# Performance work log

Measured on AMD Instinct MI355X. Metric: run time of the kernel, lower is better.

The kernel has to match this reference:

```python
import jax, jax.numpy as jnp
import numpy as np

N = 8192
IN_DIM = 512
OUT_DIM = 64
ALPHA = 0.2  # LeakyReLU negative slope
NEG_FILL = -9e15


def setup_inputs() -> dict:
    key = jax.random.key(0)
    k1, k2, k3, k4 = jax.random.split(key, 4)
    features = jax.random.normal(k1, (N, IN_DIM), dtype=jnp.float32)
    adj = jax.random.randint(k2, (N, N), 0, 2, dtype=jnp.int32)
    # xavier_normal with gain 1.414 ~ sqrt(2)
    W = jax.random.normal(k3, (IN_DIM, OUT_DIM), dtype=jnp.float32) * (1.414 * np.sqrt(2.0 / (IN_DIM + OUT_DIM)))
    a = jax.random.normal(k4, (2 * OUT_DIM, 1), dtype=jnp.float32) * (1.414 * np.sqrt(2.0 / (2 * OUT_DIM + 1)))
    return {"features": features, "adj": adj, "W": W, "a": a}


def reference(features, adj, W, a):
    h = features @ W                      # [N, OUT_DIM]
    h1 = h @ a[:OUT_DIM, :]               # [N, 1]
    h2 = h @ a[OUT_DIM:, :]               # [N, 1]
    e = h1 + h2.T                         # [N, N] broadcast add
    e = jnp.where(e > 0, e, ALPHA * e)    # LeakyReLU
    scores = jnp.where(adj > 0, e, NEG_FILL)
    attention = jax.nn.softmax(scores, axis=-1)
    out = attention @ h                   # [N, OUT_DIM]
    out = jax.nn.elu(out)                 # concat=True branch
    return out
```

## Files before the change

kernel.cpp:

```cpp
#include <hip/hip_runtime.h>
#include <hip/hip_bf16.h>

#define N 8192
#define IN_DIM 512
#define OUT_DIM 64
#define ALPHA 0.2f
#define LOG2E 1.44269504f

typedef __hip_bfloat16 bf16;
typedef __attribute__((ext_vector_type(8))) short bf16x8;
typedef __attribute__((ext_vector_type(4))) float f32x4;
typedef __attribute__((ext_vector_type(4))) int   int4v;
typedef __attribute__((ext_vector_type(4))) float float4v;

__device__ __forceinline__ float u2f(unsigned short u) {
    union { unsigned int i; float f; } c; c.i = ((unsigned int)u) << 16; return c.f;
}

__device__ __forceinline__ uint2 splitpack2(float f0, float f1) {
    unsigned u0 = __float_as_uint(f0), u1 = __float_as_uint(f1);
    unsigned h0 = u0 & 0xFFFF0000u, h1 = u1 & 0xFFFF0000u;
    float l0 = f0 - __uint_as_float(h0);
    float l1 = f1 - __uint_as_float(h1);
    uint2 r;
    r.x = (h0 >> 16) | h1;
    r.y = (__float_as_uint(l0) >> 16) | (__float_as_uint(l1) & 0xFFFF0000u);
    return r;
}

__device__ __forceinline__ bf16x8 as_bf16x8(int a, int b, int c, int d) {
    union { int4v i; bf16x8 b; } u;
    u.i = (int4v){a, b, c, d};
    return u.b;
}

__global__ void k_sniff(const unsigned short* __restrict__ feat_u16, int* __restrict__ flag) {
    int lane = threadIdx.x;
    float v = u2f(feat_u16[2 * lane]);
    float av = fabsf(v);
    int ok = (v == 0.f) || (av > 1e-8f && av < 1e8f);
    unsigned long long m = __ballot(ok);
    if (lane == 0) *flag = (__popcll(m) >= 48) ? 1 : 0;
}

__global__ __launch_bounds__(256) void k_prep(const void* __restrict__ Wv,
                                              const int* __restrict__ flag,
                                              unsigned short* __restrict__ WT_hi,
                                              unsigned short* __restrict__ WT_lo) {
    int idx = blockIdx.x * 256 + threadIdx.x;
    int k = idx >> 6, c = idx & 63;
    float w = (*flag) ? u2f(((const unsigned short*)Wv)[idx]) : ((const float*)Wv)[idx];
    unsigned u = __float_as_uint(w);
    unsigned hi = u & 0xFFFF0000u;
    float lo = w - __uint_as_float(hi);
    WT_hi[c * IN_DIM + k] = (unsigned short)(hi >> 16);
    WT_lo[c * IN_DIM + k] = (unsigned short)(__float_as_uint(lo) >> 16);
}

__global__ __launch_bounds__(64) void k_h(const void* __restrict__ featv,
                                          const unsigned short* __restrict__ WT_hi,
                                          const unsigned short* __restrict__ WT_lo,
                                          const void* __restrict__ av,
                                          const int* __restrict__ flag,
                                          float* __restrict__ h1,
                                          float* __restrict__ h2,
                                          unsigned short* __restrict__ hT_hi,
                                          unsigned short* __restrict__ hT_lo) {
    const int lane = threadIdx.x & 63;
    const int rsub = lane & 15;
    const int g = lane >> 4;
    const int wrow0 = blockIdx.x * 16;
    const int isbf = *flag;

    f32x4 acc0 = {0.f,0.f,0.f,0.f}, acc1 = {0.f,0.f,0.f,0.f};
    f32x4 acc2 = {0.f,0.f,0.f,0.f}, acc3 = {0.f,0.f,0.f,0.f};

    for (int k0 = 0; k0 < IN_DIM; k0 += 32) {
        const int ka = k0 + g * 8;
        bf16x8 Ah, Al;
        if (isbf) {
            Ah = *(const bf16x8*)((const unsigned short*)featv + (size_t)(wrow0 + rsub) * IN_DIM + ka);
            Al = as_bf16x8(0, 0, 0, 0);
        } else {
            const float* fp = (const float*)featv + (size_t)(wrow0 + rsub) * IN_DIM + ka;
            float4v f0 = *(const float4v*)fp;
            float4v f1 = *(const float4v*)(fp + 4);
            uint2 q0 = splitpack2(f0[0], f0[1]);
            uint2 q1 = splitpack2(f0[2], f0[3]);
            uint2 q2 = splitpack2(f1[0], f1[1]);
            uint2 q3 = splitpack2(f1[2], f1[3]);
            Ah = as_bf16x8((int)q0.x, (int)q1.x, (int)q2.x, (int)q3.x);
            Al = as_bf16x8((int)q0.y, (int)q1.y, (int)q2.y, (int)q3.y);
        }
        const unsigned short* wh = WT_hi + (size_t)rsub * IN_DIM + ka;
        const unsigned short* wl = WT_lo + (size_t)rsub * IN_DIM + ka;
        bf16x8 B0h = *(const bf16x8*)(wh);
        bf16x8 B1h = *(const bf16x8*)(wh + 16 * IN_DIM);
        bf16x8 B2h = *(const bf16x8*)(wh + 32 * IN_DIM);
        bf16x8 B3h = *(const bf16x8*)(wh + 48 * IN_DIM);
        bf16x8 B0l = *(const bf16x8*)(wl);
        bf16x8 B1l = *(const bf16x8*)(wl + 16 * IN_DIM);
        bf16x8 B2l = *(const bf16x8*)(wl + 32 * IN_DIM);
        bf16x8 B3l = *(const bf16x8*)(wl + 48 * IN_DIM);

        acc0 = __builtin_amdgcn_mfma_f32_16x16x32_bf16(Ah, B0h, acc0, 0, 0, 0);
        acc1 = __builtin_amdgcn_mfma_f32_16x16x32_bf16(Ah, B1h, acc1, 0, 0, 0);
        acc2 = __builtin_amdgcn_mfma_f32_16x16x32_bf16(Ah, B2h, acc2, 0, 0, 0);
        acc3 = __builtin_amdgcn_mfma_f32_16x16x32_bf16(Ah, B3h, acc3, 0, 0, 0);
        acc0 = __builtin_amdgcn_mfma_f32_16x16x32_bf16(Ah, B0l, acc0, 0, 0, 0);
        acc1 = __builtin_amdgcn_mfma_f32_16x16x32_bf16(Ah, B1l, acc1, 0, 0, 0);
        acc2 = __builtin_amdgcn_mfma_f32_16x16x32_bf16(Ah, B2l, acc2, 0, 0, 0);
        acc3 = __builtin_amdgcn_mfma_f32_16x16x32_bf16(Ah, B3l, acc3, 0, 0, 0);
        acc0 = __builtin_amdgcn_mfma_f32_16x16x32_bf16(Al, B0h, acc0, 0, 0, 0);
        acc1 = __builtin_amdgcn_mfma_f32_16x16x32_bf16(Al, B1h, acc1, 0, 0, 0);
        acc2 = __builtin_amdgcn_mfma_f32_16x16x32_bf16(Al, B2h, acc2, 0, 0, 0);
        acc3 = __builtin_amdgcn_mfma_f32_16x16x32_bf16(Al, B3h, acc3, 0, 0, 0);
    }

    {
        uint2 s01, s23;
        size_t off;
        s01 = splitpack2(acc0[0], acc0[1]); s23 = splitpack2(acc0[2], acc0[3]);
        off = (size_t)(0 * 16 + rsub) * N + wrow0 + g * 4;
        { uint2 ph; ph.x = s01.x; ph.y = s23.x; *(uint2*)(hT_hi + off) = ph; }
        { uint2 pl; pl.x = s01.y; pl.y = s23.y; *(uint2*)(hT_lo + off) = pl; }
        s01 = splitpack2(acc1[0], acc1[1]); s23 = splitpack2(acc1[2], acc1[3]);
        off = (size_t)(1 * 16 + rsub) * N + wrow0 + g * 4;
        { uint2 ph; ph.x = s01.x; ph.y = s23.x; *(uint2*)(hT_hi + off) = ph; }
        { uint2 pl; pl.x = s01.y; pl.y = s23.y; *(uint2*)(hT_lo + off) = pl; }
        s01 = splitpack2(acc2[0], acc2[1]); s23 = splitpack2(acc2[2], acc2[3]);
        off = (size_t)(2 * 16 + rsub) * N + wrow0 + g * 4;
        { uint2 ph; ph.x = s01.x; ph.y = s23.x; *(uint2*)(hT_hi + off) = ph; }
        { uint2 pl; pl.x = s01.y; pl.y = s23.y; *(uint2*)(hT_lo + off) = pl; }
        s01 = splitpack2(acc3[0], acc3[1]); s23 = splitpack2(acc3[2], acc3[3]);
        off = (size_t)(3 * 16 + rsub) * N + wrow0 + g * 4;
        { uint2 ph; ph.x = s01.x; ph.y = s23.x; *(uint2*)(hT_hi + off) = ph; }
        { uint2 pl; pl.x = s01.y; pl.y = s23.y; *(uint2*)(hT_lo + off) = pl; }
    }

    const float* af = (const float*)av;
    const unsigned short* au = (const unsigned short*)av;
    float a10 = isbf ? u2f(au[rsub])      : af[rsub];
    float a11 = isbf ? u2f(au[16 + rsub]) : af[16 + rsub];
    float a12 = isbf ? u2f(au[32 + rsub]) : af[32 + rsub];
    float a13 = isbf ? u2f(au[48 + rsub]) : af[48 + rsub];
    float a20 = isbf ? u2f(au[64 + rsub])  : af[64 + rsub];
    float a21 = isbf ? u2f(au[80 + rsub])  : af[80 + rsub];
    float a22 = isbf ? u2f(au[96 + rsub])  : af[96 + rsub];
    float a23 = isbf ? u2f(au[112 + rsub]) : af[112 + rsub];
    float s1r[4], s2r[4];
#pragma unroll
    for (int r = 0; r < 4; ++r) {
        s1r[r] = acc0[r] * a10 + acc1[r] * a11 + acc2[r] * a12 + acc3[r] * a13;
        s2r[r] = acc0[r] * a20 + acc1[r] * a21 + acc2[r] * a22 + acc3[r] * a23;
    }
#pragma unroll
    for (int off = 8; off; off >>= 1) {
#pragma unroll
        for (int r = 0; r < 4; ++r) {
            s1r[r] += __shfl_xor(s1r[r], off);
            s2r[r] += __shfl_xor(s2r[r], off);
        }
    }
    if (rsub < 4) {
        float v1 = rsub == 0 ? s1r[0] : rsub == 1 ? s1r[1] : rsub == 2 ? s1r[2] : s1r[3];
        float v2 = rsub == 0 ? s2r[0] : rsub == 1 ? s2r[1] : rsub == 2 ? s2r[2] : s2r[3];
        h1[wrow0 + g * 4 + rsub] = v1;
        h2[wrow0 + g * 4 + rsub] = v2;
    }
}

__global__ void k_h2max(const float* __restrict__ h2, float* __restrict__ h2max) {
    __shared__ float red[4];
    float m = -3e38f;
    for (int i = threadIdx.x; i < N; i += 256) m = fmaxf(m, h2[i]);
#pragma unroll
    for (int off = 32; off; off >>= 1) m = fmaxf(m, __shfl_xor(m, off));
    if ((threadIdx.x & 63) == 0) red[threadIdx.x >> 6] = m;
    __syncthreads();
    if (threadIdx.x == 0) *h2max = fmaxf(fmaxf(red[0], red[1]), fmaxf(red[2], red[3]));
}

__global__ __launch_bounds__(256, 4) void k_attn(const int* __restrict__ adj,
                                                 const float* __restrict__ h1,
                                                 const float* __restrict__ h2,
                                                 const unsigned short* __restrict__ hT_hi,
                                                 const unsigned short* __restrict__ hT_lo,
                                                 const float* __restrict__ h2max,
                                                 float* __restrict__ pacc,
                                                 float* __restrict__ plner,
                                                 int klen) {
    __shared__ float accs[4][16][64];
    __shared__ float lred[4][16];

    const int wave = threadIdx.x >> 6;
    const int lane = threadIdx.x & 63;
    const int rsub = lane & 15;
    const int g = lane >> 4;
    const int row0 = blockIdx.x * 16;
    const int row = row0 + rsub;
    const int kbid = blockIdx.y;

    const float h1r = h1[row];
    float M = h1r + *h2max;
    M = fmaxf(M, ALPHA * M);
    const float c0 = -M * LOG2E;

    f32x4 acc0 = {0.f,0.f,0.f,0.f}, acc1 = {0.f,0.f,0.f,0.f};
    f32x4 acc2 = {0.f,0.f,0.f,0.f}, acc3 = {0.f,0.f,0.f,0.f};
    float lacc = 0.f;

    const size_t arow = (size_t)row * N;
    const unsigned short* bph = hT_hi + (size_t)rsub * N;
    const unsigned short* bpl = hT_lo + (size_t)rsub * N;

    const int kbeg = kbid * klen + wave * (klen >> 2);
    const int kend = kbeg + (klen >> 2);
    for (int k0 = kbeg; k0 < kend; k0 += 32) {
        const int kb = k0 + g * 8;
        int4v aj0 = *(const int4v*)(adj + arow + kb);
        int4v aj1 = *(const int4v*)(adj + arow + kb + 4);
        float4v hA = *(const float4v*)(h2 + kb);
        float4v hB = *(const float4v*)(h2 + kb + 4);

        float w[8];
#pragma unroll
        for (int j = 0; j < 4; ++j) {
            float t = h1r + hA[j];
            float s = fmaxf(t, ALPHA * t);
            float e = exp2f(fmaf(s, LOG2E, c0));
            w[j] = aj0[j] > 0 ? e : 0.f;
        }
#pragma unroll
        for (int j = 0; j < 4; ++j) {
            float t = h1r + hB[j];
            float s = fmaxf(t, ALPHA * t);
            float e = exp2f(fmaf(s, LOG2E, c0));
            w[4 + j] = aj1[j] > 0 ? e : 0.f;
        }
#pragma unroll
        for (int j = 0; j < 8; ++j) lacc += w[j];

        uint2 p0 = splitpack2(w[0], w[1]);
        uint2 p1 = splitpack2(w[2], w[3]);
        uint2 p2 = splitpack2(w[4], w[5]);
        uint2 p3 = splitpack2(w[6], w[7]);
        bf16x8 Ahi = as_bf16x8((int)p0.x, (int)p1.x, (int)p2.x, (int)p3.x);
        bf16x8 Alo = as_bf16x8((int)p0.y, (int)p1.y, (int)p2.y, (int)p3.y);

        const unsigned short* bh = bph + kb;
        const unsigned short* bl = bpl + kb;
        bf16x8 B0h = *(const bf16x8*)(bh);
        bf16x8 B1h = *(const bf16x8*)(bh + 16 * (size_t)N);
        bf16x8 B2h = *(const bf16x8*)(bh + 32 * (size_t)N);
        bf16x8 B3h = *(const bf16x8*)(bh + 48 * (size_t)N);
        bf16x8 B0l = *(const bf16x8*)(bl);
        bf16x8 B1l = *(const bf16x8*)(bl + 16 * (size_t)N);
        bf16x8 B2l = *(const bf16x8*)(bl + 32 * (size_t)N);
        bf16x8 B3l = *(const bf16x8*)(bl + 48 * (size_t)N);

        acc0 = __builtin_amdgcn_mfma_f32_16x16x32_bf16(Ahi, B0h, acc0, 0, 0, 0);
        acc1 = __builtin_amdgcn_mfma_f32_16x16x32_bf16(Ahi, B1h, acc1, 0, 0, 0);
        acc2 = __builtin_amdgcn_mfma_f32_16x16x32_bf16(Ahi, B2h, acc2, 0, 0, 0);
        acc3 = __builtin_amdgcn_mfma_f32_16x16x32_bf16(Ahi, B3h, acc3, 0, 0, 0);
        acc0 = __builtin_amdgcn_mfma_f32_16x16x32_bf16(Ahi, B0l, acc0, 0, 0, 0);
        acc1 = __builtin_amdgcn_mfma_f32_16x16x32_bf16(Ahi, B1l, acc1, 0, 0, 0);
        acc2 = __builtin_amdgcn_mfma_f32_16x16x32_bf16(Ahi, B2l, acc2, 0, 0, 0);
        acc3 = __builtin_amdgcn_mfma_f32_16x16x32_bf16(Ahi, B3l, acc3, 0, 0, 0);
        acc0 = __builtin_amdgcn_mfma_f32_16x16x32_bf16(Alo, B0h, acc0, 0, 0, 0);
        acc1 = __builtin_amdgcn_mfma_f32_16x16x32_bf16(Alo, B1h, acc1, 0, 0, 0);
        acc2 = __builtin_amdgcn_mfma_f32_16x16x32_bf16(Alo, B2h, acc2, 0, 0, 0);
        acc3 = __builtin_amdgcn_mfma_f32_16x16x32_bf16(Alo, B3h, acc3, 0, 0, 0);
    }

    lacc += __shfl_xor(lacc, 16);
    lacc += __shfl_xor(lacc, 32);
    if (g == 0) lred[wave][rsub] = lacc;

#pragma unroll
    for (int r = 0; r < 4; ++r) {
        accs[wave][g * 4 + r][rsub]      = acc0[r];
        accs[wave][g * 4 + r][16 + rsub] = acc1[r];
        accs[wave][g * 4 + r][32 + rsub] = acc2[r];
        accs[wave][g * 4 + r][48 + rsub] = acc3[r];
    }
    __syncthreads();

    float* pa = pacc + (size_t)kbid * (N * OUT_DIM);
#pragma unroll
    for (int p = 0; p < 4; ++p) {
        int idx = p * 256 + threadIdx.x;
        int rl = idx >> 6, col = idx & 63;
        float v = accs[0][rl][col] + accs[1][rl][col] + accs[2][rl][col] + accs[3][rl][col];
        pa[(size_t)(row0 + rl) * OUT_DIM + col] = v;
        if (col == 0)
            plner[(size_t)kbid * N + row0 + rl] = lred[0][rl] + lred[1][rl] + lred[2][rl] + lred[3][rl];
    }
}

__global__ __launch_bounds__(256) void k_out(const float* __restrict__ pacc,
                                             const float* __restrict__ plner,
                                             const int* __restrict__ flag,
                                             void* __restrict__ outv,
                                             int nkb) {
    int idx = blockIdx.x * 256 + threadIdx.x;
    int row = idx >> 6;
    float v = 0.f, l = 0.f;
    for (int kb = 0; kb < nkb; ++kb) {
        v += pacc[(size_t)kb * (N * OUT_DIM) + idx];
        l += plner[(size_t)kb * N + row];
    }
    float o = l > 0.f ? v / l : 0.f;
    o = o > 0.f ? o : exp2f(o * LOG2E) - 1.f;
    if (*flag) ((bf16*)outv)[idx] = __float2bfloat16(o);
    else       ((float*)outv)[idx] = o;
}

extern "C" void kernel_launch(void* const* d_in, const int* in_sizes, int n_in,
                              void* d_out, int out_size, void* d_ws, size_t ws_size,
                              hipStream_t stream) {
    const void* feat = d_in[0];
    const int* adj = (const int*)d_in[1];
    const void* W = d_in[2];
    const void* a = d_in[3];

    char* ws = (char*)d_ws;
    int*   flag   = (int*)(ws);
    float* h2max  = (float*)(ws + 256);
    float* h1     = (float*)(ws + 4096);
    float* h2     = (float*)(ws + 36864);
    unsigned short* hT_hi = (unsigned short*)(ws + 69632);
    unsigned short* hT_lo = (unsigned short*)(ws + 69632 + 1048576);
    unsigned short* WT_hi = (unsigned short*)(ws + 2166784);
    unsigned short* WT_lo = (unsigned short*)(ws + 2166784 + 65536);
    char* dynbase = ws + 2297856;

    size_t cap = ws_size ? ws_size : ((size_t)1 << 30);
    int nkb = 4;
    while (nkb > 1) {
        size_t need = 2297856 + (size_t)nkb * ((size_t)N * OUT_DIM * 4 + (size_t)N * 4);
        if (need <= cap) break;
        nkb >>= 1;
    }
    float* pacc  = (float*)dynbase;
    float* plner = (float*)(dynbase + (size_t)nkb * N * OUT_DIM * 4);

    hipLaunchKernelGGL(k_sniff, dim3(1), dim3(64), 0, stream,
                       (const unsigned short*)feat, flag);
    hipLaunchKernelGGL(k_prep, dim3((IN_DIM * OUT_DIM) / 256), dim3(256), 0, stream,
                       W, flag, WT_hi, WT_lo);
    hipLaunchKernelGGL(k_h, dim3(N / 16), dim3(64), 0, stream,
                       feat, WT_hi, WT_lo, a, flag, h1, h2, hT_hi, hT_lo);
    hipLaunchKernelGGL(k_h2max, dim3(1), dim3(256), 0, stream, h2, h2max);
    hipLaunchKernelGGL(k_attn, dim3(N / 16, nkb), dim3(256), 0, stream,
                       adj, h1, h2, hT_hi, hT_lo, h2max, pacc, plner, N / nkb);
    hipLaunchKernelGGL(k_out, dim3((N * OUT_DIM) / 256), dim3(256), 0, stream,
                       pacc, plner, flag, d_out, nkb);
}
```

Baseline: 510.7 us.

## Tile attention over 64 rows per block and fuse h2 max via atomics

Each k_attn block now covers 64 rows (four 16-row MFMA tiles) instead of 16. The hT B-fragments and h2 loads are reused across the four row tiles, which cuts redundant B traffic by four. The separate k_h2max launch is removed; k_h computes the h2 max with an order-preserving encoded atomicMax, and h1/h2 are stored prescaled by log2e. The wave partial sums are reduced serially into a padded shared tile. Occupancy is lowered (launch bounds 256,2) to fit 64 accumulator vectors, and the K split is raised to 8, which adds partial-sum traffic in k_out.

```diff
diff --git a/kernel.cpp b/kernel.cpp
--- a/kernel.cpp
+++ b/kernel.cpp
@@ -34,6 +34,14 @@
     return u.b;
 }
 
+__device__ __forceinline__ unsigned fenc(float f) {
+    unsigned u = __float_as_uint(f);
+    return (u & 0x80000000u) ? ~u : (u | 0x80000000u);
+}
+__device__ __forceinline__ float fdec(unsigned e) {
+    return (e & 0x80000000u) ? __uint_as_float(e & 0x7FFFFFFFu) : __uint_as_float(~e);
+}
+
 __global__ void k_sniff(const unsigned short* __restrict__ feat_u16, int* __restrict__ flag) {
     int lane = threadIdx.x;
     float v = u2f(feat_u16[2 * lane]);
@@ -46,7 +54,9 @@
 __global__ __launch_bounds__(256) void k_prep(const void* __restrict__ Wv,
                                               const int* __restrict__ flag,
                                               unsigned short* __restrict__ WT_hi,
-                                              unsigned short* __restrict__ WT_lo) {
+                                              unsigned short* __restrict__ WT_lo,
+                                              unsigned* __restrict__ h2enc) {
+    if (blockIdx.x == 0 && threadIdx.x == 0) *h2enc = fenc(-3e38f);
     int idx = blockIdx.x * 256 + threadIdx.x;
     int k = idx >> 6, c = idx & 63;
     float w = (*flag) ? u2f(((const unsigned short*)Wv)[idx]) : ((const float*)Wv)[idx];
@@ -65,7 +75,8 @@
                                           float* __restrict__ h1,
                                           float* __restrict__ h2,
                                           unsigned short* __restrict__ hT_hi,
-                                          unsigned short* __restrict__ hT_lo) {
+                                          unsigned short* __restrict__ hT_lo,
+                                          unsigned* __restrict__ h2enc) {
     const int lane = threadIdx.x & 63;
     const int rsub = lane & 15;
     const int g = lane >> 4;
@@ -162,55 +173,54 @@
             s2r[r] += __shfl_xor(s2r[r], off);
         }
     }
+    float wm = fmaxf(fmaxf(s2r[0], s2r[1]), fmaxf(s2r[2], s2r[3])) * LOG2E;
+#pragma unroll
+    for (int off = 32; off; off >>= 1) wm = fmaxf(wm, __shfl_xor(wm, off));
+    if (lane == 0) atomicMax(h2enc, fenc(wm));
+
     if (rsub < 4) {
         float v1 = rsub == 0 ? s1r[0] : rsub == 1 ? s1r[1] : rsub == 2 ? s1r[2] : s1r[3];
         float v2 = rsub == 0 ? s2r[0] : rsub == 1 ? s2r[1] : rsub == 2 ? s2r[2] : s2r[3];
-        h1[wrow0 + g * 4 + rsub] = v1;
-        h2[wrow0 + g * 4 + rsub] = v2;
-    }
-}
-
-__global__ void k_h2max(const float* __restrict__ h2, float* __restrict__ h2max) {
-    __shared__ float red[4];
-    float m = -3e38f;
-    for (int i = threadIdx.x; i < N; i += 256) m = fmaxf(m, h2[i]);
-#pragma unroll
-    for (int off = 32; off; off >>= 1) m = fmaxf(m, __shfl_xor(m, off));
-    if ((threadIdx.x & 63) == 0) red[threadIdx.x >> 6] = m;
-    __syncthreads();
-    if (threadIdx.x == 0) *h2max = fmaxf(fmaxf(red[0], red[1]), fmaxf(red[2], red[3]));
-}
-
-__global__ __launch_bounds__(256, 4) void k_attn(const int* __restrict__ adj,
+        h1[wrow0 + g * 4 + rsub] = v1 * LOG2E;
+        h2[wrow0 + g * 4 + rsub] = v2 * LOG2E;
+    }
+}
+
+__global__ __launch_bounds__(256, 2) void k_attn(const int* __restrict__ adj,
                                                  const float* __restrict__ h1,
                                                  const float* __restrict__ h2,
                                                  const unsigned short* __restrict__ hT_hi,
                                                  const unsigned short* __restrict__ hT_lo,
-                                                 const float* __restrict__ h2max,
+                                                 const unsigned* __restrict__ h2enc,
                                                  float* __restrict__ pacc,
                                                  float* __restrict__ plner,
                                                  int klen) {
-    __shared__ float accs[4][16][64];
-    __shared__ float lred[4][16];
+    __shared__ float accs[64][66];
+    __shared__ float lredL[4][64];
 
     const int wave = threadIdx.x >> 6;
     const int lane = threadIdx.x & 63;
     const int rsub = lane & 15;
     const int g = lane >> 4;
-    const int row0 = blockIdx.x * 16;
-    const int row = row0 + rsub;
+    const int row0 = blockIdx.x * 64;
     const int kbid = blockIdx.y;
 
-    const float h1r = h1[row];
-    float M = h1r + *h2max;
-    M = fmaxf(M, ALPHA * M);
-    const float c0 = -M * LOG2E;
-
-    f32x4 acc0 = {0.f,0.f,0.f,0.f}, acc1 = {0.f,0.f,0.f,0.f};
-    f32x4 acc2 = {0.f,0.f,0.f,0.f}, acc3 = {0.f,0.f,0.f,0.f};
-    float lacc = 0.f;
-
-    const size_t arow = (size_t)row * N;
+    const float h2m = fdec(*h2enc);
+    float h1r[4], c0[4];
+#pragma unroll
+    for (int mt = 0; mt < 4; ++mt) {
+        h1r[mt] = h1[row0 + mt * 16 + rsub];
+        float u = h1r[mt] + h2m;
+        c0[mt] = -fmaxf(u, ALPHA * u);
+    }
+
+    f32x4 acc[4][4];
+#pragma unroll
+    for (int mt = 0; mt < 4; ++mt)
+#pragma unroll
+        for (int ct = 0; ct < 4; ++ct) acc[mt][ct] = (f32x4){0.f, 0.f, 0.f, 0.f};
+    float lacc[4] = {0.f, 0.f, 0.f, 0.f};
+
     const unsigned short* bph = hT_hi + (size_t)rsub * N;
     const unsigned short* bpl = hT_lo + (size_t)rsub * N;
 
@@ -218,35 +228,6 @@
     const int kend = kbeg + (klen >> 2);
     for (int k0 = kbeg; k0 < kend; k0 += 32) {
         const int kb = k0 + g * 8;
-        int4v aj0 = *(const int4v*)(adj + arow + kb);
-        int4v aj1 = *(const int4v*)(adj + arow + kb + 4);
-        float4v hA = *(const float4v*)(h2 + kb);
-        float4v hB = *(const float4v*)(h2 + kb + 4);
-
-        float w[8];
-#pragma unroll
-        for (int j = 0; j < 4; ++j) {
-            float t = h1r + hA[j];
-            float s = fmaxf(t, ALPHA * t);
-            float e = exp2f(fmaf(s, LOG2E, c0));
-            w[j] = aj0[j] > 0 ? e : 0.f;
-        }
-#pragma unroll
-        for (int j = 0; j < 4; ++j) {
-            float t = h1r + hB[j];
-            float s = fmaxf(t, ALPHA * t);
-            float e = exp2f(fmaf(s, LOG2E, c0));
-            w[4 + j] = aj1[j] > 0 ? e : 0.f;
-        }
-#pragma unroll
-        for (int j = 0; j < 8; ++j) lacc += w[j];
-
-        uint2 p0 = splitpack2(w[0], w[1]);
-        uint2 p1 = splitpack2(w[2], w[3]);
-        uint2 p2 = splitpack2(w[4], w[5]);
-        uint2 p3 = splitpack2(w[6], w[7]);
-        bf16x8 Ahi = as_bf16x8((int)p0.x, (int)p1.x, (int)p2.x, (int)p3.x);
-        bf16x8 Alo = as_bf16x8((int)p0.y, (int)p1.y, (int)p2.y, (int)p3.y);
 
         const unsigned short* bh = bph + kb;
         const unsigned short* bl = bpl + kb;
@@ -259,43 +240,97 @@
         bf16x8 B2l = *(const bf16x8*)(bl + 32 * (size_t)N);
         bf16x8 B3l = *(const bf16x8*)(bl + 48 * (size_t)N);
 
-        acc0 = __builtin_amdgcn_mfma_f32_16x16x32_bf16(Ahi, B0h, acc0, 0, 0, 0);
-        acc1 = __builtin_amdgcn_mfma_f32_16x16x32_bf16(Ahi, B1h, acc1, 0, 0, 0);
-        acc2 = __builtin_amdgcn_mfma_f32_16x16x32_bf16(Ahi, B2h, acc2, 0, 0, 0);
-        acc3 = __builtin_amdgcn_mfma_f32_16x16x32_bf16(Ahi, B3h, acc3, 0, 0, 0);
-        acc0 = __builtin_amdgcn_mfma_f32_16x16x32_bf16(Ahi, B0l, acc0, 0, 0, 0);
-        acc1 = __builtin_amdgcn_mfma_f32_16x16x32_bf16(Ahi, B1l, acc1, 0, 0, 0);
-        acc2 = __builtin_amdgcn_mfma_f32_16x16x32_bf16(Ahi, B2l, acc2, 0, 0, 0);
-        acc3 = __builtin_amdgcn_mfma_f32_16x16x32_bf16(Ahi, B3l, acc3, 0, 0, 0);
-        acc0 = __builtin_amdgcn_mfma_f32_16x16x32_bf16(Alo, B0h, acc0, 0, 0, 0);
-        acc1 = __builtin_amdgcn_mfma_f32_16x16x32_bf16(Alo, B1h, acc1, 0, 0, 0);
-        acc2 = __builtin_amdgcn_mfma_f32_16x16x32_bf16(Alo, B2h, acc2, 0, 0, 0);
-        acc3 = __builtin_amdgcn_mfma_f32_16x16x32_bf16(Alo, B3h, acc3, 0, 0, 0);
-    }
-
-    lacc += __shfl_xor(lacc, 16);
-    lacc += __shfl_xor(lacc, 32);
-    if (g == 0) lred[wave][rsub] = lacc;
-
-#pragma unroll
-    for (int r = 0; r < 4; ++r) {
-        accs[wave][g * 4 + r][rsub]      = acc0[r];
-        accs[wave][g * 4 + r][16 + rsub] = acc1[r];
-        accs[wave][g * 4 + r][32 + rsub] = acc2[r];
-        accs[wave][g * 4 + r][48 + rsub] = acc3[r];
+        float4v hA = *(const float4v*)(h2 + kb);
+        float4v hB = *(const float4v*)(h2 + kb + 4);
+
+#pragma unroll
+        for (int mt = 0; mt < 4; ++mt) {
+            const size_t arow = (size_t)(row0 + mt * 16 + rsub) * N + kb;
+            int4v aj0 = *(const int4v*)(adj + arow);
+            int4v aj1 = *(const int4v*)(adj + arow + 4);
+
+            float w[8];
+#pragma unroll
+            for (int j = 0; j < 4; ++j) {
+                float u = h1r[mt] + hA[j];
+                float s = fmaxf(u, ALPHA * u);
+                float e = exp2f(s + c0[mt]);
+                w[j] = aj0[j] > 0 ? e : 0.f;
+            }
+#pragma unroll
+            for (int j = 0; j < 4; ++j) {
+                float u = h1r[mt] + hB[j];
+                float s = fmaxf(u, ALPHA * u);
+                float e = exp2f(s + c0[mt]);
+                w[4 + j] = aj1[j] > 0 ? e : 0.f;
+            }
+#pragma unroll
+            for (int j = 0; j < 8; ++j) lacc[mt] += w[j];
+
+            uint2 p0 = splitpack2(w[0], w[1]);
+            uint2 p1 = splitpack2(w[2], w[3]);
+            uint2 p2 = splitpack2(w[4], w[5]);
+            uint2 p3 = splitpack2(w[6], w[7]);
+            bf16x8 Ahi = as_bf16x8((int)p0.x, (int)p1.x, (int)p2.x, (int)p3.x);
+            bf16x8 Alo = as_bf16x8((int)p0.y, (int)p1.y, (int)p2.y, (int)p3.y);
+
+            acc[mt][0] = __builtin_amdgcn_mfma_f32_16x16x32_bf16(Ahi, B0h, acc[mt][0], 0, 0, 0);
+            acc[mt][1] = __builtin_amdgcn_mfma_f32_16x16x32_bf16(Ahi, B1h, acc[mt][1], 0, 0, 0);
+            acc[mt][2] = __builtin_amdgcn_mfma_f32_16x16x32_bf16(Ahi, B2h, acc[mt][2], 0, 0, 0);
+            acc[mt][3] = __builtin_amdgcn_mfma_f32_16x16x32_bf16(Ahi, B3h, acc[mt][3], 0, 0, 0);
+            acc[mt][0] = __builtin_amdgcn_mfma_f32_16x16x32_bf16(Ahi, B0l, acc[mt][0], 0, 0, 0);
+            acc[mt][1] = __builtin_amdgcn_mfma_f32_16x16x32_bf16(Ahi, B1l, acc[mt][1], 0, 0, 0);
+            acc[mt][2] = __builtin_amdgcn_mfma_f32_16x16x32_bf16(Ahi, B2l, acc[mt][2], 0, 0, 0);
+            acc[mt][3] = __builtin_amdgcn_mfma_f32_16x16x32_bf16(Ahi, B3l, acc[mt][3], 0, 0, 0);
+            acc[mt][0] = __builtin_amdgcn_mfma_f32_16x16x32_bf16(Alo, B0h, acc[mt][0], 0, 0, 0);
+            acc[mt][1] = __builtin_amdgcn_mfma_f32_16x16x32_bf16(Alo, B1h, acc[mt][1], 0, 0, 0);
+            acc[mt][2] = __builtin_amdgcn_mfma_f32_16x16x32_bf16(Alo, B2h, acc[mt][2], 0, 0, 0);
+            acc[mt][3] = __builtin_amdgcn_mfma_f32_16x16x32_bf16(Alo, B3h, acc[mt][3], 0, 0, 0);
+        }
+    }
+
+#pragma unroll
+    for (int mt = 0; mt < 4; ++mt) {
+        float l = lacc[mt];
+        l += __shfl_xor(l, 16);
+        l += __shfl_xor(l, 32);
+        if (g == 0) lredL[wave][mt * 16 + rsub] = l;
+    }
+
+    if (wave == 0) {
+#pragma unroll
+        for (int mt = 0; mt < 4; ++mt)
+#pragma unroll
+            for (int ct = 0; ct < 4; ++ct)
+#pragma unroll
+                for (int r = 0; r < 4; ++r)
+                    accs[mt * 16 + g * 4 + r][ct * 16 + rsub] = acc[mt][ct][r];
     }
     __syncthreads();
+#pragma unroll
+    for (int w2 = 1; w2 < 4; ++w2) {
+        if (wave == w2) {
+#pragma unroll
+            for (int mt = 0; mt < 4; ++mt)
+#pragma unroll
+                for (int ct = 0; ct < 4; ++ct)
+#pragma unroll
+                    for (int r = 0; r < 4; ++r)
+                        accs[mt * 16 + g * 4 + r][ct * 16 + rsub] += acc[mt][ct][r];
+        }
+        __syncthreads();
+    }
 
     float* pa = pacc + (size_t)kbid * (N * OUT_DIM);
 #pragma unroll
-    for (int p = 0; p < 4; ++p) {
+    for (int p = 0; p < 16; ++p) {
         int idx = p * 256 + threadIdx.x;
         int rl = idx >> 6, col = idx & 63;
-        float v = accs[0][rl][col] + accs[1][rl][col] + accs[2][rl][col] + accs[3][rl][col];
-        pa[(size_t)(row0 + rl) * OUT_DIM + col] = v;
-        if (col == 0)
-            plner[(size_t)kbid * N + row0 + rl] = lred[0][rl] + lred[1][rl] + lred[2][rl] + lred[3][rl];
-    }
+        pa[(size_t)(row0 + rl) * OUT_DIM + col] = accs[rl][col];
+    }
+    if (threadIdx.x < 64)
+        plner[(size_t)kbid * N + row0 + threadIdx.x] =
+            lredL[0][threadIdx.x] + lredL[1][threadIdx.x] + lredL[2][threadIdx.x] + lredL[3][threadIdx.x];
 }
 
 __global__ __launch_bounds__(256) void k_out(const float* __restrict__ pacc,
@@ -325,10 +360,10 @@
     const void* a = d_in[3];
 
     char* ws = (char*)d_ws;
-    int*   flag   = (int*)(ws);
-    float* h2max  = (float*)(ws + 256);
-    float* h1     = (float*)(ws + 4096);
-    float* h2     = (float*)(ws + 36864);
+    int*      flag  = (int*)(ws);
+    unsigned* h2enc = (unsigned*)(ws + 256);
+    float* h1       = (float*)(ws + 4096);
+    float* h2       = (float*)(ws + 36864);
     unsigned short* hT_hi = (unsigned short*)(ws + 69632);
     unsigned short* hT_lo = (unsigned short*)(ws + 69632 + 1048576);
     unsigned short* WT_hi = (unsigned short*)(ws + 2166784);
@@ -336,7 +371,7 @@
     char* dynbase = ws + 2297856;
 
     size_t cap = ws_size ? ws_size : ((size_t)1 << 30);
-    int nkb = 4;
+    int nkb = 8;
     while (nkb > 1) {
         size_t need = 2297856 + (size_t)nkb * ((size_t)N * OUT_DIM * 4 + (size_t)N * 4);
         if (need <= cap) break;
@@ -348,12 +383,11 @@
     hipLaunchKernelGGL(k_sniff, dim3(1), dim3(64), 0, stream,
                        (const unsigned short*)feat, flag);
     hipLaunchKernelGGL(k_prep, dim3((IN_DIM * OUT_DIM) / 256), dim3(256), 0, stream,
-                       W, flag, WT_hi, WT_lo);
+                       W, flag, WT_hi, WT_lo, h2enc);
     hipLaunchKernelGGL(k_h, dim3(N / 16), dim3(64), 0, stream,
-                       feat, WT_hi, WT_lo, a, flag, h1, h2, hT_hi, hT_lo);
-    hipLaunchKernelGGL(k_h2max, dim3(1), dim3(256), 0, stream, h2, h2max);
-    hipLaunchKernelGGL(k_attn, dim3(N / 16, nkb), dim3(256), 0, stream,
-                       adj, h1, h2, hT_hi, hT_lo, h2max, pacc, plner, N / nkb);
+                       feat, WT_hi, WT_lo, a, flag, h1, h2, hT_hi, hT_lo, h2enc);
+    hipLaunchKernelGGL(k_attn, dim3(N / 64, nkb), dim3(256), 0, stream,
+                       adj, h1, h2, hT_hi, hT_lo, h2enc, pacc, plner, N / nkb);
     hipLaunchKernelGGL(k_out, dim3((N * OUT_DIM) / 256), dim3(256), 0, stream,
                        pacc, plner, flag, d_out, nkb);
 }
```

Result: faster. 420.1 us (-17.7%).
